# Performance work log

Measured on AMD Instinct MI355X. Metric: run time of the kernel, lower is better.

The kernel has to match this reference:

```python
import jax, jax.numpy as jnp
import numpy as np

B, T, IN, HID, LAT = 256, 512, 128, 64, 16

def _mk_lstm(key, in_dim, h_dim, scale):
    k1, k2, k3, k4 = jax.random.split(key, 4)
    return (jax.random.normal(k1, (4 * h_dim, in_dim), jnp.float32) * scale,
            jax.random.normal(k2, (4 * h_dim, h_dim), jnp.float32) * scale,
            jax.random.normal(k3, (4 * h_dim,), jnp.float32) * scale,
            jax.random.normal(k4, (4 * h_dim,), jnp.float32) * scale)

def setup_inputs() -> dict:
    key = jax.random.key(0)
    ks = jax.random.split(key, 5)
    x = jax.random.normal(ks[0], (B, T, IN), jnp.float32)
    out = {"x": x}
    dims = [(IN, HID, "e1"), (HID, LAT, "e2"), (LAT, HID, "d1"), (HID, IN, "d2")]
    for k, (di, dh, nm) in zip(ks[1:], dims):
        scale = 1.0 / np.sqrt(dh)  # pytorch LSTM init range ~ 1/sqrt(hidden)
        Wih, Whh, bih, bhh = _mk_lstm(k, di, dh, scale)
        out[f"Wih_{nm}"], out[f"Whh_{nm}"], out[f"bih_{nm}"], out[f"bhh_{nm}"] = Wih, Whh, bih, bhh
    return out

def lstm(x, Wih, Whh, bih, bhh):
    # x: [B,T,I]; gates ordered i,f,g,o as in torch.nn.LSTM
    H = Whh.shape[1]
    xg = jnp.einsum('bti,gi->btg', x, Wih) + bih + bhh  # [B,T,4H]
    def step(carry, xt):
        h, c = carry
        g = xt + h @ Whh.T
        i, f, gg, o = jnp.split(g, 4, axis=-1)
        c = jax.nn.sigmoid(f) * c + jax.nn.sigmoid(i) * jnp.tanh(gg)
        h = jax.nn.sigmoid(o) * jnp.tanh(c)
        return (h, c), h
    b = x.shape[0]
    h0 = jnp.zeros((b, H), x.dtype)
    _, hs = jax.lax.scan(step, (h0, h0), jnp.swapaxes(xg, 0, 1))
    return jnp.swapaxes(hs, 0, 1)  # [B,T,H]

def reference(x, Wih_e1, Whh_e1, bih_e1, bhh_e1, Wih_e2, Whh_e2, bih_e2, bhh_e2,
              Wih_d1, Whh_d1, bih_d1, bhh_d1, Wih_d2, Whh_d2, bih_d2, bhh_d2):
    # dropout layers are identity at inference
    out = jax.nn.relu(lstm(x, Wih_e1, Whh_e1, bih_e1, bhh_e1))
    out = jax.nn.relu(lstm(out, Wih_e2, Whh_e2, bih_e2, bhh_e2))
    latent = out[:, -1, :]                                  # [B,LAT]
    dec_in = jnp.broadcast_to(latent[:, None, :], (x.shape[0], x.shape[1], latent.shape[-1]))
    out = jax.nn.relu(lstm(dec_in, Wih_d1, Whh_d1, bih_d1, bhh_d1))
    return lstm(out, Wih_d2, Whh_d2, bih_d2, bhh_d2)        # [B,T,IN]
```

## Files before the change

kernel.cpp:

```cpp
#include <hip/hip_runtime.h>


#define BB 256
#define TT 512

typedef _Float16 half2v __attribute__((ext_vector_type(2)));

static __device__ __forceinline__ float dot2(half2v a, half2v b, float c){
  return __builtin_amdgcn_fdot2(a,b,c,false);
}
static __device__ __forceinline__ float qsum1(float v){
  int t = __builtin_amdgcn_update_dpp(0, __float_as_int(v), 0xB1, 0xF, 0xF, true);
  return v + __int_as_float(t);
}
static __device__ __forceinline__ float qsum2(float v){
  int t = __builtin_amdgcn_update_dpp(0, __float_as_int(v), 0x4E, 0xF, 0xF, true);
  return v + __int_as_float(t);
}
template<int CTRL>
static __device__ __forceinline__ float qb(float v){
  return __int_as_float(__builtin_amdgcn_update_dpp(0, __float_as_int(v), CTRL, 0xF, 0xF, true));
}
static __device__ __forceinline__ unsigned packh2(float lo, float hi){
  half2v p; p.x=(_Float16)lo; p.y=(_Float16)hi;
  return __builtin_bit_cast(unsigned, p);
}
static __device__ __forceinline__ half2v ash2(unsigned u){ return __builtin_bit_cast(half2v,u); }
static __device__ __forceinline__ half2v mkh2(float lo, float hi){
  half2v p; p.x=(_Float16)lo; p.y=(_Float16)hi; return p;
}

static __device__ __forceinline__ float lstm_update(int q, float a0, float a1,
                                                    float a2, float a3, float& c){
  float mine = a0;
  mine = (q==1) ? a1 : mine;
  mine = (q==2) ? a2 : mine;
  mine = (q==3) ? a3 : mine;
  const bool isg = (q==2);
  const float arg = isg ? (mine+mine) : mine;
  const float s   = 1.0f/(1.0f + __expf(-arg));
  const float act = isg ? (s+s-1.0f) : s;
  const float bi = qb<0x00>(act);
  const float bf = qb<0x55>(act);
  const float bg = qb<0xAA>(act);
  const float bo = qb<0xFF>(act);
  c = bf*c + bi*bg;
  const float s2 = 1.0f/(1.0f + __expf(-(c+c)));
  return bo*(s2+s2-1.0f);
}

__global__ void __launch_bounds__(512, 2) k_fused(
    const float* __restrict__ x,
    const float* __restrict__ WihE1, const float* __restrict__ WhhE1,
    const float* __restrict__ bihE1, const float* __restrict__ bhhE1,
    const float* __restrict__ WihE2, const float* __restrict__ WhhE2,
    const float* __restrict__ bihE2, const float* __restrict__ bhhE2,
    const float* __restrict__ WihD1, const float* __restrict__ WhhD1,
    const float* __restrict__ bihD1, const float* __restrict__ bhhD1,
    const float* __restrict__ WihD2, const float* __restrict__ WhhD2,
    const float* __restrict__ bihD2, const float* __restrict__ bhhD2,
    float* __restrict__ out)
{
  const int b = blockIdx.x, tid = threadIdx.x;

  __shared__ unsigned vhE [2*96];
  __shared__ unsigned e2op[2*48];
  __shared__ unsigned dop [2*96];
  __shared__ unsigned vhD1[2*32];
  __shared__ float    latF[16];

  {
    const int q = tid & 3, j = tid >> 2;
    const bool e1act = (tid < 256);
    half2v w1[4][24];
    float bias1[4] = {0.f,0.f,0.f,0.f};
    if (e1act){
#pragma unroll
      for (int g=0; g<4; ++g){
        const int row = g*64 + j;
        bias1[g] = (q==0) ? (bihE1[row]+bhhE1[row]) : 0.0f;
#pragma unroll
        for (int m=0;m<24;++m){
          const int k0 = 48*q + 2*m;
          const float lo = (k0   < 128)? WihE1[row*128+k0]   : WhhE1[row*64 + (k0-128)];
          const float hi = (k0+1 < 128)? WihE1[row*128+k0+1] : WhhE1[row*64 + (k0+1-128)];
          w1[g][m] = mkh2(lo,hi);
        }
      }
    }
    const bool e2act = (tid >= 256 && tid < 320);
    const int q2 = tid & 3, j2 = (tid - 256) >> 2;
    half2v w2[4][12];
    float bias2[4] = {0.f,0.f,0.f,0.f};
    if (e2act){
#pragma unroll
      for (int g=0; g<4; ++g){
        const int row = g*16 + j2;
        bias2[g] = (q2==0) ? (bihE2[row]+bhhE2[row]) : 0.0f;
#pragma unroll
        for (int m=0;m<12;++m){
          const int k0 = 24*q2 + 2*m;
          float lo = 0.0f, hi = 0.0f;
          if (k0 < 64)        lo = WihE2[row*64+k0];
          else if (k0 < 80)   lo = WhhE2[row*16 + (k0-64)];
          if (k0+1 < 64)      hi = WihE2[row*64+k0+1];
          else if (k0+1 < 80) hi = WhhE2[row*16 + (k0+1-64)];
          w2[g][m] = mkh2(lo,hi);
        }
      }
    }
    const bool xact = (tid >= 448);
    const int  xl   = tid - 448;
    const float* xrow = x + (size_t)b * (TT*128);
    float2 xa, xb;
    if (xact){
      float2 v0 = *(const float2*)(xrow + 2*xl);
      vhE[xl] = packh2(v0.x, v0.y);
      xa = *(const float2*)(xrow + 1*128 + 2*xl);
      xb = *(const float2*)(xrow + 2*128 + 2*xl);
    }
    if (tid >= 64 && tid < 96)   vhE[64 + (tid-64)] = 0u;
    if (tid >= 96 && tid < 192)  e2op[tid-96] = 0u;
    float c1 = 0.0f, c2 = 0.0f;
    __syncthreads();

    for (int t = 0; t <= TT; ++t){
      const int cur = t & 1, nxt = cur ^ 1;
      if (t < TT && e1act){
        float a0=bias1[0], a1=bias1[1], a2=bias1[2], a3=bias1[3];
        const uint4* vp = (const uint4*)(vhE + cur*96 + q*24);
#pragma unroll
        for (int r=0;r<6;++r){
          const uint4 u = vp[r];
          const half2v o0=ash2(u.x), o1=ash2(u.y), o2=ash2(u.z), o3=ash2(u.w);
          a0=dot2(w1[0][4*r+0],o0,a0); a1=dot2(w1[1][4*r+0],o0,a1);
          a2=dot2(w1[2][4*r+0],o0,a2); a3=dot2(w1[3][4*r+0],o0,a3);
          a0=dot2(w1[0][4*r+1],o1,a0); a1=dot2(w1[1][4*r+1],o1,a1);
          a2=dot2(w1[2][4*r+1],o1,a2); a3=dot2(w1[3][4*r+1],o1,a3);
          a0=dot2(w1[0][4*r+2],o2,a0); a1=dot2(w1[1][4*r+2],o2,a1);
          a2=dot2(w1[2][4*r+2],o2,a2); a3=dot2(w1[3][4*r+2],o2,a3);
          a0=dot2(w1[0][4*r+3],o3,a0); a1=dot2(w1[1][4*r+3],o3,a1);
          a2=dot2(w1[2][4*r+3],o3,a2); a3=dot2(w1[3][4*r+3],o3,a3);
        }
        a0=qsum2(qsum1(a0)); a1=qsum2(qsum1(a1));
        a2=qsum2(qsum1(a2)); a3=qsum2(qsum1(a3));
        const float h = lstm_update(q, a0, a1, a2, a3, c1);
        if (q == 0){
          ((_Float16*)(vhE + nxt*96))[128 + j] = (_Float16)h;
          ((_Float16*)(e2op + cur*48))[j]      = (_Float16)fmaxf(h, 0.0f);
        }
      }
      if (t < TT && xact){
        vhE[nxt*96 + xl] = packh2(xa.x, xa.y);
        xa = xb;
        const int t3 = (t+3 < TT) ? (t+3) : (TT-1);
        xb = *(const float2*)(xrow + (size_t)t3*128 + 2*xl);
      }
      if (t >= 1 && e2act){
        const int t2 = t-1, c2p = t2 & 1, n2p = c2p ^ 1;
        float a0=bias2[0], a1=bias2[1], a2=bias2[2], a3=bias2[3];
        const uint4* vp = (const uint4*)(e2op + c2p*48 + q2*12);
#pragma unroll
        for (int r=0;r<3;++r){
          const uint4 u = vp[r];
          const half2v o0=ash2(u.x), o1=ash2(u.y), o2=ash2(u.z), o3=ash2(u.w);
          a0=dot2(w2[0][4*r+0],o0,a0); a1=dot2(w2[1][4*r+0],o0,a1);
          a2=dot2(w2[2][4*r+0],o0,a2); a3=dot2(w2[3][4*r+0],o0,a3);
          a0=dot2(w2[0][4*r+1],o1,a0); a1=dot2(w2[1][4*r+1],o1,a1);
          a2=dot2(w2[2][4*r+1],o1,a2); a3=dot2(w2[3][4*r+1],o1,a3);
          a0=dot2(w2[0][4*r+2],o2,a0); a1=dot2(w2[1][4*r+2],o2,a1);
          a2=dot2(w2[2][4*r+2],o2,a2); a3=dot2(w2[3][4*r+2],o2,a3);
          a0=dot2(w2[0][4*r+3],o3,a0); a1=dot2(w2[1][4*r+3],o3,a1);
          a2=dot2(w2[2][4*r+3],o3,a2); a3=dot2(w2[3][4*r+3],o3,a3);
        }
        a0=qsum2(qsum1(a0)); a1=qsum2(qsum1(a1));
        a2=qsum2(qsum1(a2)); a3=qsum2(qsum1(a3));
        const float h = lstm_update(q2, a0, a1, a2, a3, c2);
        if (q2 == 0){
          ((_Float16*)(e2op + n2p*48))[64 + j2] = (_Float16)h;
          if (t2 == TT-1) latF[j2] = fmaxf(h, 0.0f);
        }
      }
      __syncthreads();
    }
  }
  __syncthreads();

  {
    const int qd = tid & 3, jd = tid >> 2;
    half2v wD2[4][24];
    float biasD2[4];
#pragma unroll
    for (int g=0; g<4; ++g){
      const int row = g*128 + jd;
      biasD2[g] = (qd==0)? (bihD2[row]+bhhD2[row]) : 0.0f;
#pragma unroll
      for (int m=0;m<24;++m){
        const int k0 = 48*qd + 2*m;
        const float lo = (k0   < 64)? WihD2[row*64+k0]   : WhhD2[row*128+(k0-64)];
        const float hi = (k0+1 < 64)? WihD2[row*64+k0+1] : WhhD2[row*128+(k0+1-64)];
        wD2[g][m] = mkh2(lo,hi);
      }
    }
    const bool d1act = (tid < 256);
    half2v wD1[4][8];
    float projD1[4] = {0.f,0.f,0.f,0.f};
    if (d1act){
#pragma unroll
      for (int g=0; g<4; ++g){
        const int row = g*64 + jd;
#pragma unroll
        for (int m=0;m<8;++m){
          const int k0 = 16*qd + 2*m;
          wD1[g][m] = mkh2(WhhD1[row*64+k0], WhhD1[row*64+k0+1]);
        }
        if (qd==0){
          float a = bihD1[row]+bhhD1[row];
#pragma unroll
          for (int i=0;i<16;++i) a = fmaf(WihD1[row*16+i], latF[i], a);
          projD1[g] = a;
        }
      }
    }
    if (tid < 192)               dop[tid] = 0u;
    if (tid >= 192 && tid < 224) vhD1[tid-192] = 0u;
    float cd1 = 0.0f, cd2 = 0.0f;
    float* orow = out + (size_t)b * (TT*128);
    __syncthreads();

    for (int t = 0; t <= TT; ++t){
      const int cur = t & 1;
      if (t < TT && d1act){
        const int nxt = cur ^ 1;
        float a0=projD1[0], a1=projD1[1], a2=projD1[2], a3=projD1[3];
        const uint4* vp = (const uint4*)(vhD1 + cur*32 + qd*8);
#pragma unroll
        for (int r=0;r<2;++r){
          const uint4 u = vp[r];
          const half2v o0=ash2(u.x),o1=ash2(u.y),o2=ash2(u.z),o3=ash2(u.w);
          a0=dot2(wD1[0][4*r+0],o0,a0); a1=dot2(wD1[1][4*r+0],o0,a1);
          a2=dot2(wD1[2][4*r+0],o0,a2); a3=dot2(wD1[3][4*r+0],o0,a3);
          a0=dot2(wD1[0][4*r+1],o1,a0); a1=dot2(wD1[1][4*r+1],o1,a1);
          a2=dot2(wD1[2][4*r+1],o1,a2); a3=dot2(wD1[3][4*r+1],o1,a3);
          a0=dot2(wD1[0][4*r+2],o2,a0); a1=dot2(wD1[1][4*r+2],o2,a1);
          a2=dot2(wD1[2][4*r+2],o2,a2); a3=dot2(wD1[3][4*r+2],o2,a3);
          a0=dot2(wD1[0][4*r+3],o3,a0); a1=dot2(wD1[1][4*r+3],o3,a1);
          a2=dot2(wD1[2][4*r+3],o3,a2); a3=dot2(wD1[3][4*r+3],o3,a3);
        }
        a0=qsum2(qsum1(a0)); a1=qsum2(qsum1(a1));
        a2=qsum2(qsum1(a2)); a3=qsum2(qsum1(a3));
        const float h = lstm_update(qd, a0, a1, a2, a3, cd1);
        if (qd==0){
          ((_Float16*)(vhD1 + nxt*32))[jd] = (_Float16)h;
          ((_Float16*)(dop + cur*96))[jd]  = (_Float16)fmaxf(h,0.0f);
        }
      }
      if (t >= 1){
        const int t2 = t-1, c2p = t2 & 1, n2p = c2p ^ 1;
        float a0=biasD2[0], a1=biasD2[1], a2=biasD2[2], a3=biasD2[3];
        const uint4* vp = (const uint4*)(dop + c2p*96 + qd*24);
#pragma unroll
        for (int r=0;r<6;++r){
          const uint4 u = vp[r];
          const half2v o0=ash2(u.x),o1=ash2(u.y),o2=ash2(u.z),o3=ash2(u.w);
          a0=dot2(wD2[0][4*r+0],o0,a0); a1=dot2(wD2[1][4*r+0],o0,a1);
          a2=dot2(wD2[2][4*r+0],o0,a2); a3=dot2(wD2[3][4*r+0],o0,a3);
          a0=dot2(wD2[0][4*r+1],o1,a0); a1=dot2(wD2[1][4*r+1],o1,a1);
          a2=dot2(wD2[2][4*r+1],o1,a2); a3=dot2(wD2[3][4*r+1],o1,a3);
          a0=dot2(wD2[0][4*r+2],o2,a0); a1=dot2(wD2[1][4*r+2],o2,a1);
          a2=dot2(wD2[2][4*r+2],o2,a2); a3=dot2(wD2[3][4*r+2],o2,a3);
          a0=dot2(wD2[0][4*r+3],o3,a0); a1=dot2(wD2[1][4*r+3],o3,a1);
          a2=dot2(wD2[2][4*r+3],o3,a2); a3=dot2(wD2[3][4*r+3],o3,a3);
        }
        a0=qsum2(qsum1(a0)); a1=qsum2(qsum1(a1));
        a2=qsum2(qsum1(a2)); a3=qsum2(qsum1(a3));
        const float h = lstm_update(qd, a0, a1, a2, a3, cd2);
        if (qd==0){
          ((_Float16*)(dop + n2p*96))[64 + jd] = (_Float16)h;
          orow[(size_t)t2*128 + jd] = h;
        }
      }
      __syncthreads();
    }
  }
}

extern "C" void kernel_launch(void* const* d_in, const int* in_sizes, int n_in,
                              void* d_out, int out_size, void* d_ws, size_t ws_size,
                              hipStream_t stream) {
  const float* x      = (const float*)d_in[0];
  const float* WihE1  = (const float*)d_in[1];
  const float* WhhE1  = (const float*)d_in[2];
  const float* bihE1  = (const float*)d_in[3];
  const float* bhhE1  = (const float*)d_in[4];
  const float* WihE2  = (const float*)d_in[5];
  const float* WhhE2  = (const float*)d_in[6];
  const float* bihE2  = (const float*)d_in[7];
  const float* bhhE2  = (const float*)d_in[8];
  const float* WihD1  = (const float*)d_in[9];
  const float* WhhD1  = (const float*)d_in[10];
  const float* bihD1  = (const float*)d_in[11];
  const float* bhhD1  = (const float*)d_in[12];
  const float* WihD2  = (const float*)d_in[13];
  const float* WhhD2  = (const float*)d_in[14];
  const float* bihD2  = (const float*)d_in[15];
  const float* bhhD2  = (const float*)d_in[16];
  float* out = (float*)d_out;

  k_fused<<<BB, 512, 0, stream>>>(x,
      WihE1, WhhE1, bihE1, bhhE1,
      WihE2, WhhE2, bihE2, bhhE2,
      WihD1, WhhD1, bihD1, bhhD1,
      WihD2, WhhD2, bihD2, bhhD2,
      out);
}
```

Measured before the change: 838.8 us.

## Spread encoder layer across all threads and split decoder into sequential phases

```diff
diff --git a/kernel.cpp b/kernel.cpp
--- a/kernel.cpp
+++ b/kernel.cpp
@@ -8,18 +8,15 @@
 
 static __device__ __forceinline__ float dot2(half2v a, half2v b, float c){
   return __builtin_amdgcn_fdot2(a,b,c,false);
-}
-static __device__ __forceinline__ float qsum1(float v){
-  int t = __builtin_amdgcn_update_dpp(0, __float_as_int(v), 0xB1, 0xF, 0xF, true);
-  return v + __int_as_float(t);
-}
-static __device__ __forceinline__ float qsum2(float v){
-  int t = __builtin_amdgcn_update_dpp(0, __float_as_int(v), 0x4E, 0xF, 0xF, true);
-  return v + __int_as_float(t);
 }
 template<int CTRL>
 static __device__ __forceinline__ float qb(float v){
   return __int_as_float(__builtin_amdgcn_update_dpp(0, __float_as_int(v), CTRL, 0xF, 0xF, true));
+}
+static __device__ __forceinline__ float qsum1(float v){ return v + qb<0xB1>(v); }
+static __device__ __forceinline__ float qsum2(float v){ return v + qb<0x4E>(v); }
+static __device__ __forceinline__ float hsum8(float v){
+  v = qsum1(v); v = qsum2(v); return v + qb<0x141>(v);
 }
 static __device__ __forceinline__ unsigned packh2(float lo, float hi){
   half2v p; p.x=(_Float16)lo; p.y=(_Float16)hi;
@@ -63,33 +60,31 @@
 {
   const int b = blockIdx.x, tid = threadIdx.x;
 
+  __shared__ unsigned hbuf[TT*32];
   __shared__ unsigned vhE [2*96];
-  __shared__ unsigned e2op[2*48];
-  __shared__ unsigned dop [2*96];
+  __shared__ unsigned h2r [2*16];
   __shared__ unsigned vhD1[2*32];
+  __shared__ unsigned drng[2*64];
   __shared__ float    latF[16];
 
   {
-    const int q = tid & 3, j = tid >> 2;
-    const bool e1act = (tid < 256);
-    half2v w1[4][24];
-    float bias1[4] = {0.f,0.f,0.f,0.f};
-    if (e1act){
-#pragma unroll
-      for (int g=0; g<4; ++g){
-        const int row = g*64 + j;
-        bias1[g] = (q==0) ? (bihE1[row]+bhhE1[row]) : 0.0f;
-#pragma unroll
-        for (int m=0;m<24;++m){
-          const int k0 = 48*q + 2*m;
-          const float lo = (k0   < 128)? WihE1[row*128+k0]   : WhhE1[row*64 + (k0-128)];
-          const float hi = (k0+1 < 128)? WihE1[row*128+k0+1] : WhhE1[row*64 + (k0+1-128)];
-          w1[g][m] = mkh2(lo,hi);
-        }
-      }
-    }
-    const bool e2act = (tid >= 256 && tid < 320);
-    const int q2 = tid & 3, j2 = (tid - 256) >> 2;
+    const int o = tid & 7, j = tid >> 3;
+    half2v w1[4][12];
+    float bias1[4];
+#pragma unroll
+    for (int g=0; g<4; ++g){
+      const int row = g*64 + j;
+      bias1[g] = (o==0) ? (bihE1[row]+bhhE1[row]) : 0.0f;
+#pragma unroll
+      for (int m=0;m<12;++m){
+        const int k0 = 24*o + 2*m;
+        const float lo = (k0   < 128)? WihE1[row*128+k0]   : WhhE1[row*64 + (k0-128)];
+        const float hi = (k0+1 < 128)? WihE1[row*128+k0+1] : WhhE1[row*64 + (k0+1-128)];
+        w1[g][m] = mkh2(lo,hi);
+      }
+    }
+    const bool e2act = (tid >= 64 && tid < 128);
+    const int q2 = tid & 3, j2 = (tid - 64) >> 2;
     half2v w2[4][12];
     float bias2[4] = {0.f,0.f,0.f,0.f};
     if (e2act){
@@ -109,28 +104,33 @@
         }
       }
     }
-    const bool xact = (tid >= 448);
-    const int  xl   = tid - 448;
+    const bool xact = (tid < 64);
     const float* xrow = x + (size_t)b * (TT*128);
     float2 xa, xb;
     if (xact){
-      float2 v0 = *(const float2*)(xrow + 2*xl);
-      vhE[xl] = packh2(v0.x, v0.y);
-      xa = *(const float2*)(xrow + 1*128 + 2*xl);
-      xb = *(const float2*)(xrow + 2*128 + 2*xl);
-    }
-    if (tid >= 64 && tid < 96)   vhE[64 + (tid-64)] = 0u;
-    if (tid >= 96 && tid < 192)  e2op[tid-96] = 0u;
+      float2 v0 = *(const float2*)(xrow + 2*tid);
+      vhE[tid] = packh2(v0.x, v0.y);
+      xa = *(const float2*)(xrow + 128 + 2*tid);
+      xb = *(const float2*)(xrow + 256 + 2*tid);
+    }
+    if (tid >= 128 && tid < 160) vhE[64 + (tid-128)] = 0u;
+    if (tid >= 160 && tid < 192) h2r[tid-160] = 0u;
     float c1 = 0.0f, c2 = 0.0f;
     __syncthreads();
 
     for (int t = 0; t <= TT; ++t){
       const int cur = t & 1, nxt = cur ^ 1;
-      if (t < TT && e1act){
+      if (t < TT && xact){
+        vhE[nxt*96 + tid] = packh2(xa.x, xa.y);
+        xa = xb;
+        const int t3 = (t+3 < TT) ? (t+3) : (TT-1);
+        xb = *(const float2*)(xrow + (size_t)t3*128 + 2*tid);
+      }
+      if (t < TT){
         float a0=bias1[0], a1=bias1[1], a2=bias1[2], a3=bias1[3];
-        const uint4* vp = (const uint4*)(vhE + cur*96 + q*24);
-#pragma unroll
-        for (int r=0;r<6;++r){
+        const uint4* vp = (const uint4*)(vhE + cur*96 + o*12);
+#pragma unroll
+        for (int r=0;r<3;++r){
           const uint4 u = vp[r];
           const half2v o0=ash2(u.x), o1=ash2(u.y), o2=ash2(u.z), o3=ash2(u.w);
           a0=dot2(w1[0][4*r+0],o0,a0); a1=dot2(w1[1][4*r+0],o0,a1);
@@ -142,27 +142,21 @@
           a0=dot2(w1[0][4*r+3],o3,a0); a1=dot2(w1[1][4*r+3],o3,a1);
           a2=dot2(w1[2][4*r+3],o3,a2); a3=dot2(w1[3][4*r+3],o3,a3);
         }
-        a0=qsum2(qsum1(a0)); a1=qsum2(qsum1(a1));
-        a2=qsum2(qsum1(a2)); a3=qsum2(qsum1(a3));
-        const float h = lstm_update(q, a0, a1, a2, a3, c1);
-        if (q == 0){
+        a0=hsum8(a0); a1=hsum8(a1); a2=hsum8(a2); a3=hsum8(a3);
+        const float h = lstm_update(o & 3, a0, a1, a2, a3, c1);
+        if (o == 0){
           ((_Float16*)(vhE + nxt*96))[128 + j] = (_Float16)h;
-          ((_Float16*)(e2op + cur*48))[j]      = (_Float16)fmaxf(h, 0.0f);
-        }
-      }
-      if (t < TT && xact){
-        vhE[nxt*96 + xl] = packh2(xa.x, xa.y);
-        xa = xb;
-        const int t3 = (t+3 < TT) ? (t+3) : (TT-1);
-        xb = *(const float2*)(xrow + (size_t)t3*128 + 2*xl);
+          ((_Float16*)(hbuf + t*32))[j]        = (_Float16)fmaxf(h, 0.0f);
+        }
       }
       if (t >= 1 && e2act){
-        const int t2 = t-1, c2p = t2 & 1, n2p = c2p ^ 1;
+        const int t2 = t-1, cp = t2 & 1, np = cp ^ 1;
         float a0=bias2[0], a1=bias2[1], a2=bias2[2], a3=bias2[3];
-        const uint4* vp = (const uint4*)(e2op + c2p*48 + q2*12);
 #pragma unroll
         for (int r=0;r<3;++r){
-          const uint4 u = vp[r];
+          const int d = q2*12 + 4*r;
+          const unsigned* p = (d < 32) ? (hbuf + t2*32 + d) : (h2r + cp*16 + (d-32));
+          const uint4 u = *(const uint4*)p;
           const half2v o0=ash2(u.x), o1=ash2(u.y), o2=ash2(u.z), o3=ash2(u.w);
           a0=dot2(w2[0][4*r+0],o0,a0); a1=dot2(w2[1][4*r+0],o0,a1);
           a2=dot2(w2[2][4*r+0],o0,a2); a3=dot2(w2[3][4*r+0],o0,a3);
@@ -177,7 +171,7 @@
         a2=qsum2(qsum1(a2)); a3=qsum2(qsum1(a3));
         const float h = lstm_update(q2, a0, a1, a2, a3, c2);
         if (q2 == 0){
-          ((_Float16*)(e2op + n2p*48))[64 + j2] = (_Float16)h;
+          ((_Float16*)(h2r + np*16))[j2] = (_Float16)h;
           if (t2 == TT-1) latF[j2] = fmaxf(h, 0.0f);
         }
       }
@@ -185,27 +179,14 @@
     }
   }
   __syncthreads();
+  asm volatile("" ::: "memory");
 
   {
+    const bool act = (tid < 256);
     const int qd = tid & 3, jd = tid >> 2;
-    half2v wD2[4][24];
-    float biasD2[4];
-#pragma unroll
-    for (int g=0; g<4; ++g){
-      const int row = g*128 + jd;
-      biasD2[g] = (qd==0)? (bihD2[row]+bhhD2[row]) : 0.0f;
-#pragma unroll
-      for (int m=0;m<24;++m){
-        const int k0 = 48*qd + 2*m;
-        const float lo = (k0   < 64)? WihD2[row*64+k0]   : WhhD2[row*128+(k0-64)];
-        const float hi = (k0+1 < 64)? WihD2[row*64+k0+1] : WhhD2[row*128+(k0+1-64)];
-        wD2[g][m] = mkh2(lo,hi);
-      }
-    }
-    const bool d1act = (tid < 256);
     half2v wD1[4][8];
     float projD1[4] = {0.f,0.f,0.f,0.f};
-    if (d1act){
+    if (act){
 #pragma unroll
       for (int g=0; g<4; ++g){
         const int row = g*64 + jd;
@@ -222,16 +203,13 @@
         }
       }
     }
-    if (tid < 192)               dop[tid] = 0u;
-    if (tid >= 192 && tid < 224) vhD1[tid-192] = 0u;
-    float cd1 = 0.0f, cd2 = 0.0f;
-    float* orow = out + (size_t)b * (TT*128);
+    if (tid < 32) vhD1[tid] = 0u;
+    float cd1 = 0.0f;
     __syncthreads();
 
-    for (int t = 0; t <= TT; ++t){
-      const int cur = t & 1;
-      if (t < TT && d1act){
-        const int nxt = cur ^ 1;
+    for (int t = 0; t < TT; ++t){
+      const int cur = t & 1, nxt = cur ^ 1;
+      if (act){
         float a0=projD1[0], a1=projD1[1], a2=projD1[2], a3=projD1[3];
         const uint4* vp = (const uint4*)(vhD1 + cur*32 + qd*8);
 #pragma unroll
@@ -252,33 +230,60 @@
         const float h = lstm_update(qd, a0, a1, a2, a3, cd1);
         if (qd==0){
           ((_Float16*)(vhD1 + nxt*32))[jd] = (_Float16)h;
-          ((_Float16*)(dop + cur*96))[jd]  = (_Float16)fmaxf(h,0.0f);
-        }
-      }
-      if (t >= 1){
-        const int t2 = t-1, c2p = t2 & 1, n2p = c2p ^ 1;
-        float a0=biasD2[0], a1=biasD2[1], a2=biasD2[2], a3=biasD2[3];
-        const uint4* vp = (const uint4*)(dop + c2p*96 + qd*24);
-#pragma unroll
-        for (int r=0;r<6;++r){
-          const uint4 u = vp[r];
-          const half2v o0=ash2(u.x),o1=ash2(u.y),o2=ash2(u.z),o3=ash2(u.w);
-          a0=dot2(wD2[0][4*r+0],o0,a0); a1=dot2(wD2[1][4*r+0],o0,a1);
-          a2=dot2(wD2[2][4*r+0],o0,a2); a3=dot2(wD2[3][4*r+0],o0,a3);
-          a0=dot2(wD2[0][4*r+1],o1,a0); a1=dot2(wD2[1][4*r+1],o1,a1);
-          a2=dot2(wD2[2][4*r+1],o1,a2); a3=dot2(wD2[3][4*r+1],o1,a3);
-          a0=dot2(wD2[0][4*r+2],o2,a0); a1=dot2(wD2[1][4*r+2],o2,a1);
-          a2=dot2(wD2[2][4*r+2],o2,a2); a3=dot2(wD2[3][4*r+2],o2,a3);
-          a0=dot2(wD2[0][4*r+3],o3,a0); a1=dot2(wD2[1][4*r+3],o3,a1);
-          a2=dot2(wD2[2][4*r+3],o3,a2); a3=dot2(wD2[3][4*r+3],o3,a3);
-        }
-        a0=qsum2(qsum1(a0)); a1=qsum2(qsum1(a1));
-        a2=qsum2(qsum1(a2)); a3=qsum2(qsum1(a3));
-        const float h = lstm_update(qd, a0, a1, a2, a3, cd2);
-        if (qd==0){
-          ((_Float16*)(dop + n2p*96))[64 + jd] = (_Float16)h;
-          orow[(size_t)t2*128 + jd] = h;
-        }
+          ((_Float16*)(hbuf + t*32))[jd]   = (_Float16)fmaxf(h,0.0f);
+        }
+      }
+      __syncthreads();
+    }
+  }
+  __syncthreads();
+  asm volatile("" ::: "memory");
+
+  {
+    const int qd = tid & 3, jd = tid >> 2;
+    half2v wD2[4][24];
+    float biasD2[4];
+#pragma unroll
+    for (int g=0; g<4; ++g){
+      const int row = g*128 + jd;
+      biasD2[g] = (qd==0)? (bihD2[row]+bhhD2[row]) : 0.0f;
+#pragma unroll
+      for (int m=0;m<24;++m){
+        const int k0 = 48*qd + 2*m;
+        const float lo = (k0   < 64)? WihD2[row*64+k0]   : WhhD2[row*128+(k0-64)];
+        const float hi = (k0+1 < 64)? WihD2[row*64+k0+1] : WhhD2[row*128+(k0+1-64)];
+        wD2[g][m] = mkh2(lo,hi);
+      }
+    }
+    if (tid < 64) drng[tid] = 0u;
+    float cd2 = 0.0f;
+    float* orow = out + (size_t)b * (TT*128);
+    __syncthreads();
+
+    for (int t = 0; t < TT; ++t){
+      const int cur = t & 1, nxt = cur ^ 1;
+      float a0=biasD2[0], a1=biasD2[1], a2=biasD2[2], a3=biasD2[3];
+#pragma unroll
+      for (int r=0;r<6;++r){
+        const int d = qd*24 + 4*r;
+        const unsigned* p = (d < 32) ? (hbuf + t*32 + d) : (drng + cur*64 + (d-32));
+        const uint4 u = *(const uint4*)p;
+        const half2v o0=ash2(u.x),o1=ash2(u.y),o2=ash2(u.z),o3=ash2(u.w);
+        a0=dot2(wD2[0][4*r+0],o0,a0); a1=dot2(wD2[1][4*r+0],o0,a1);
+        a2=dot2(wD2[2][4*r+0],o0,a2); a3=dot2(wD2[3][4*r+0],o0,a3);
+        a0=dot2(wD2[0][4*r+1],o1,a0); a1=dot2(wD2[1][4*r+1],o1,a1);
+        a2=dot2(wD2[2][4*r+1],o1,a2); a3=dot2(wD2[3][4*r+1],o1,a3);
+        a0=dot2(wD2[0][4*r+2],o2,a0); a1=dot2(wD2[1][4*r+2],o2,a1);
+        a2=dot2(wD2[2][4*r+2],o2,a2); a3=dot2(wD2[3][4*r+2],o2,a3);
+        a0=dot2(wD2[0][4*r+3],o3,a0); a1=dot2(wD2[1][4*r+3],o3,a1);
+        a2=dot2(wD2[2][4*r+3],o3,a2); a3=dot2(wD2[3][4*r+3],o3,a3);
+      }
+      a0=qsum2(qsum1(a0)); a1=qsum2(qsum1(a1));
+      a2=qsum2(qsum1(a2)); a3=qsum2(qsum1(a3));
+      const float h = lstm_update(qd, a0, a1, a2, a3, cd2);
+      if (qd==0){
+        ((_Float16*)(drng + nxt*64))[jd] = (_Float16)h;
+        orow[(size_t)t*128 + jd] = h;
       }
       __syncthreads();
     }
```

Result: slower. 995.9 us (+18.7%).
